# Optimization experiments

Hardware: AMD Instinct MI355X
Metric: run time of the kernel (lower is better)

Reference implementation:

```python
import jax, jax.numpy as jnp
import numpy as np

STRIDES = (2, 2, 1)   # module init arg: (2,2,1) per docstring example
EPS = 1e-5            # InstanceNorm epsilon
ALPHA = 0.2           # leaky relu slope
DN = ('NDHWC', 'DHWIO', 'NDHWC')


def setup_inputs() -> dict:
    key = jax.random.key(0)
    k1, k2 = jax.random.split(key, 2)
    # x: [B, D, H, W, Cin] NDHWC volume batch
    x = jax.random.normal(k1, (4, 128, 128, 32, 32), dtype=jnp.float32)
    # w: per-sample hypernetwork kernels [B, kD, kH, kW, Cin, Cout]
    w = jax.random.normal(k2, (4, 3, 3, 3, 32, 64), dtype=jnp.float32) * 0.05
    # InstanceNorm affine params (learned)
    gamma = jnp.ones((64,), dtype=jnp.float32)
    beta = jnp.zeros((64,), dtype=jnp.float32)
    return {"x": x, "w": w, "gamma": gamma, "beta": beta}


def _per_sample_conv(xi, wi):
    # xi: [D,H,W,Cin], wi: [kD,kH,kW,Cin,Cout] -> [D',H',W',Cout]
    return jax.lax.conv_general_dilated(
        xi[None], wi, window_strides=STRIDES, padding='SAME',
        dimension_numbers=DN)[0]


def reference(x, w, gamma, beta):
    # batched dynamic conv: distinct kernel per sample, vectorized via vmap
    y = jax.vmap(_per_sample_conv)(x, w)          # [B, D', H', W', Cout]
    # InstanceNorm: normalize over spatial dims per sample, per channel
    mu = jnp.mean(y, axis=(1, 2, 3), keepdims=True)
    var = jnp.var(y, axis=(1, 2, 3), keepdims=True)
    y = (y - mu) * jax.lax.rsqrt(var + EPS) * gamma + beta
    # leaky relu alpha=0.2
    return jnp.where(y >= 0, y, ALPHA * y)
```

## Files before the change

kernel.cpp:

```cpp
#include <hip/hip_runtime.h>
#include <hip/hip_bf16.h>

#define B_ 4
#define D_ 128
#define H_ 128
#define W_ 32
#define CI 32
#define CO 64
#define OD 64
#define OH 64
#define OW 32
#define S_SPATIAL (OD*OH*OW)
#define EPS 1e-5f
#define ALPHA 0.2f

#define XR 9
#define XC 34
#define UNITS (4*XR*XC)
#define XSLICEB (UNITS*16)
#define WSLICEB (9*4096)
#define PLANEF (H_*W_*CI)

typedef __attribute__((ext_vector_type(8))) short short8;
typedef __attribute__((ext_vector_type(4))) float f32x4;

__device__ inline short f2bf(float f) {
    return __builtin_bit_cast(short, __float2bfloat16(f));
}

__device__ inline short8 pack8(float4 a, float4 b) {
    short8 r;
    r[0]=f2bf(a.x); r[1]=f2bf(a.y); r[2]=f2bf(a.z); r[3]=f2bf(a.w);
    r[4]=f2bf(b.x); r[5]=f2bf(b.y); r[6]=f2bf(b.z); r[7]=f2bf(b.w);
    return r;
}

__device__ inline void gload16(const void* g, const void* l) {
    __builtin_amdgcn_global_load_lds(
        (const __attribute__((address_space(1))) void*)g,
        (__attribute__((address_space(3))) void*)l, 16, 0, 0);
}

__global__ __launch_bounds__(512) void zero_ws_kernel(float* ws) {
    ws[threadIdx.x] = 0.f;
}

__global__ __launch_bounds__(64) void wprep_kernel(const float* __restrict__ w,
                                                   short* __restrict__ wp) {
    int blk = blockIdx.x;
    int nf  = blk & 3;
    int tb  = blk >> 2;
    int l   = threadIdx.x;
    int l15 = l & 15, lhi = l >> 4;
    const float* wsrc = w + (size_t)tb * (CI*CO);
    short8 v;
#pragma unroll
    for (int j = 0; j < 8; ++j)
        v[j] = f2bf(wsrc[(lhi*8 + j)*CO + nf*16 + l15]);
    *(short8*)(wp + (size_t)blk*512 + l*8) = v;
}

#define BARRIER_FULL() \
    asm volatile("s_waitcnt vmcnt(0) lgkmcnt(0)" ::: "memory"); \
    __builtin_amdgcn_s_barrier(); \
    __builtin_amdgcn_sched_barrier(0)

#define BARRIER_LGKM() \
    asm volatile("s_waitcnt lgkmcnt(0)" ::: "memory"); \
    __builtin_amdgcn_s_barrier(); \
    __builtin_amdgcn_sched_barrier(0)

__global__ __launch_bounds__(256, 2) void conv_mfma_kernel(const float* __restrict__ x,
                                                           const short* __restrict__ wp,
                                                           float* __restrict__ out,
                                                           float* __restrict__ ws) {
    const int bid = blockIdx.x;
    const int b   = bid >> 10;
    const int od  = (bid >> 4) & 63;
    const int oh0 = (bid & 15) << 2;
    const int t   = threadIdx.x;
    const int wv  = t >> 6;
    const int l   = t & 63;
    const int l15 = l & 15;
    const int lhi = l >> 4;

    const float* xb  = x + (size_t)b * (D_*PLANEF);
    const short* wpb = wp + (size_t)b * (27*2048);

    __shared__ __align__(16) char smem[XSLICEB + WSLICEB];
    char* xbuf = smem;
    char* wbuf = smem + XSLICEB;

    int soff[5];
#pragma unroll
    for (int k = 0; k < 5; ++k) {
        int U   = t + (k << 8);
        int g   = U / (XR*XC);
        int rem = U % (XR*XC);
        int r   = rem / XC;
        int c   = rem % XC;
        int ih  = oh0*2 + r;
        int iw  = c - 1;
        soff[k] = (U < UNITS && ih < H_ && (unsigned)iw < (unsigned)W_)
                    ? (ih*(W_*CI) + iw*CI + g*8) : -1;
    }

    f32x4 acc[2][4];
#pragma unroll
    for (int mf = 0; mf < 2; ++mf)
#pragma unroll
        for (int nf = 0; nf < 4; ++nf)
            acc[mf][nf] = (f32x4){0.f, 0.f, 0.f, 0.f};

    auto stage = [&](const float* plane, int kd) {
        const short* wsrc = wpb + (size_t)kd * (9*2048);
#pragma unroll
        for (int k = 0; k < 9; ++k) {
            int u = t + (k << 8);
            gload16(wsrc + u*8, wbuf + u*16);
        }
        float4 la[5], lb[5];
#pragma unroll
        for (int k = 0; k < 5; ++k) {
            if (soff[k] >= 0) {
                la[k] = *(const float4*)(plane + soff[k]);
                lb[k] = *(const float4*)(plane + soff[k] + 4);
            } else {
                la[k] = make_float4(0.f,0.f,0.f,0.f);
                lb[k] = la[k];
            }
        }
#pragma unroll
        for (int k = 0; k < 5; ++k) {
            int U = t + (k << 8);
            if (U < UNITS) *(short8*)(xbuf + U*16) = pack8(la[k], lb[k]);
        }
    };

    auto compute = [&]() {
#pragma unroll
        for (int kh = 0; kh < 3; ++kh) {
            const int r = 2*wv + kh;
#pragma unroll
            for (int kw = 0; kw < 3; ++kw) {
                const char* wpt = wbuf + (kh*3 + kw)*4096 + l*16;
                short8 bf0 = *(const short8*)(wpt);
                short8 bf1 = *(const short8*)(wpt + 1024);
                short8 bf2 = *(const short8*)(wpt + 2048);
                short8 bf3 = *(const short8*)(wpt + 3072);
#pragma unroll
                for (int mf = 0; mf < 2; ++mf) {
                    int c = mf*16 + l15 + kw;
                    int U = (lhi*XR + r)*XC + c;
                    short8 a = *(const short8*)(xbuf + U*16);
                    acc[mf][0] = __builtin_amdgcn_mfma_f32_16x16x32_bf16(a, bf0, acc[mf][0], 0,0,0);
                    acc[mf][1] = __builtin_amdgcn_mfma_f32_16x16x32_bf16(a, bf1, acc[mf][1], 0,0,0);
                    acc[mf][2] = __builtin_amdgcn_mfma_f32_16x16x32_bf16(a, bf2, acc[mf][2], 0,0,0);
                    acc[mf][3] = __builtin_amdgcn_mfma_f32_16x16x32_bf16(a, bf3, acc[mf][3], 0,0,0);
                }
            }
        }
    };

    const int id0 = od*2;
    const float* p0 = xb + (size_t)id0 * PLANEF;
    const float* p1 = p0 + PLANEF;
    const bool has2 = (id0 + 2) < D_;
    const float* p2 = has2 ? (p1 + PLANEF) : p1;

    stage(p0, 0);
    BARRIER_FULL();
    compute();
    BARRIER_LGKM();
    stage(p1, 1);
    BARRIER_FULL();
    compute();
    BARRIER_LGKM();
    stage(p2, 2);
    BARRIER_FULL();
    if (has2) compute();

    const int oh = oh0 + wv;
    float* yb = out + (size_t)((b*OD + od)*OH + oh) * (OW*CO);
#pragma unroll
    for (int mf = 0; mf < 2; ++mf)
#pragma unroll
        for (int nf = 0; nf < 4; ++nf)
#pragma unroll
            for (int r = 0; r < 4; ++r) {
                int ow = mf*16 + lhi*4 + r;
                int co = nf*16 + l15;
                yb[ow*CO + co] = acc[mf][nf][r];
            }

    __syncthreads();
    float* lsum = (float*)smem;
    float* lsq  = (float*)(smem + 1024);
    float csum[4], csq[4];
#pragma unroll
    for (int nf = 0; nf < 4; ++nf) {
        float s = 0.f, q = 0.f;
#pragma unroll
        for (int mf = 0; mf < 2; ++mf)
#pragma unroll
            for (int r = 0; r < 4; ++r) {
                float v = acc[mf][nf][r];
                s += v;
                q = fmaf(v, v, q);
            }
        s += __shfl_xor(s, 16, 64); s += __shfl_xor(s, 32, 64);
        q += __shfl_xor(q, 16, 64); q += __shfl_xor(q, 32, 64);
        csum[nf] = s; csq[nf] = q;
    }
    if (lhi == 0) {
#pragma unroll
        for (int nf = 0; nf < 4; ++nf) {
            lsum[wv*64 + nf*16 + l15] = csum[nf];
            lsq[wv*64 + nf*16 + l15]  = csq[nf];
        }
    }
    __syncthreads();
    if (t < 64) {
        float s = lsum[t] + lsum[64 + t] + lsum[128 + t] + lsum[192 + t];
        float q = lsq[t]  + lsq[64 + t]  + lsq[128 + t]  + lsq[192 + t];
        atomicAdd(&ws[b*64 + t], s);
        atomicAdd(&ws[256 + b*64 + t], q);
    }
}

__global__ __launch_bounds__(256) void finalize_kernel(float* ws,
                                                       const float* __restrict__ gamma,
                                                       const float* __restrict__ beta) {
    int t = threadIdx.x;
    int co = t & 63;
    const float invS = 1.0f / (float)S_SPATIAL;
    float sum = ws[t];
    float sq  = ws[256 + t];
    float mu  = sum * invS;
    float var = sq * invS - mu*mu;
    float scale = rsqrtf(var + EPS) * gamma[co];
    ws[512 + t] = scale;
    ws[768 + t] = beta[co] - mu*scale;
}

__global__ __launch_bounds__(256) void norm_kernel(float* __restrict__ y,
                                                   const float* __restrict__ ws) {
    size_t i = (size_t)blockIdx.x * 256 + threadIdx.x;
    int b = (int)(i >> 21);
    const float4* scp = (const float4*)(ws + 512 + b*64);
    const float4* shp = (const float4*)(ws + 768 + b*64);
    float4 sc = scp[i & 15];
    float4 sh = shp[i & 15];
    float4 v = ((const float4*)y)[i];
    float4 r;
    r.x = fmaf(v.x, sc.x, sh.x);
    r.y = fmaf(v.y, sc.y, sh.y);
    r.z = fmaf(v.z, sc.z, sh.z);
    r.w = fmaf(v.w, sc.w, sh.w);
    r.x = r.x >= 0.f ? r.x : ALPHA * r.x;
    r.y = r.y >= 0.f ? r.y : ALPHA * r.y;
    r.z = r.z >= 0.f ? r.z : ALPHA * r.z;
    r.w = r.w >= 0.f ? r.w : ALPHA * r.w;
    ((float4*)y)[i] = r;
}

extern "C" void kernel_launch(void* const* d_in, const int* in_sizes, int n_in,
                              void* d_out, int out_size, void* d_ws, size_t ws_size,
                              hipStream_t stream) {
    const float* x     = (const float*)d_in[0];
    const float* w     = (const float*)d_in[1];
    const float* gamma = (const float*)d_in[2];
    const float* beta  = (const float*)d_in[3];
    float* out = (float*)d_out;
    float* ws  = (float*)d_ws;
    short* wp  = (short*)((char*)d_ws + 4096);

    zero_ws_kernel<<<1, 512, 0, stream>>>(ws);
    wprep_kernel<<<B_*27*4, 64, 0, stream>>>(w, wp);
    conv_mfma_kernel<<<B_*OD*(OH/4), 256, 0, stream>>>(x, wp, out, ws);
    finalize_kernel<<<1, 256, 0, stream>>>(ws, gamma, beta);
    norm_kernel<<<32768, 256, 0, stream>>>(out, ws);
}
```

Before: 242.4 us.

## Overlap async x-plane DMA with MFMA compute via raw LDS staging and double buffering

Input planes are now fetched with asynchronous global-to-LDS loads of raw fp32 rows into an XOR-swizzled buffer. They are then repacked to bf16 in LDS, double-buffered so the next plane's DMA overlaps the current plane's MFMA work. Weight fragments are read straight from global/L2 instead of being staged through LDS. This hides global load latency behind compute, at the cost of more LDS, possibly lower occupancy, and per-iteration global weight reads.

New measurement: 232.2 us. 4.2% less time.

```diff
diff --git a/kernel.cpp b/kernel.cpp
--- a/kernel.cpp
+++ b/kernel.cpp
@@ -17,9 +17,10 @@
 #define XR 9
 #define XC 34
 #define UNITS (4*XR*XC)
-#define XSLICEB (UNITS*16)
-#define WSLICEB (9*4096)
-#define PLANEF (H_*W_*CI)
+#define BFSLICE (UNITS*16)
+#define ROWF 1024
+#define RAWB (XR*ROWF*4)
+#define PLANEF (H_*ROWF)
 
 typedef __attribute__((ext_vector_type(8))) short short8;
 typedef __attribute__((ext_vector_type(4))) float f32x4;
@@ -60,12 +61,12 @@
     *(short8*)(wp + (size_t)blk*512 + l*8) = v;
 }
 
-#define BARRIER_FULL() \
+#define BAR_VM0() \
     asm volatile("s_waitcnt vmcnt(0) lgkmcnt(0)" ::: "memory"); \
     __builtin_amdgcn_s_barrier(); \
     __builtin_amdgcn_sched_barrier(0)
 
-#define BARRIER_LGKM() \
+#define BAR_LGKM() \
     asm volatile("s_waitcnt lgkmcnt(0)" ::: "memory"); \
     __builtin_amdgcn_s_barrier(); \
     __builtin_amdgcn_sched_barrier(0)
@@ -87,23 +88,43 @@
     const float* xb  = x + (size_t)b * (D_*PLANEF);
     const short* wpb = wp + (size_t)b * (27*2048);
 
-    __shared__ __align__(16) char smem[XSLICEB + WSLICEB];
-    char* xbuf = smem;
-    char* wbuf = smem + XSLICEB;
-
-    int soff[5];
-#pragma unroll
-    for (int k = 0; k < 5; ++k) {
-        int U   = t + (k << 8);
-        int g   = U / (XR*XC);
-        int rem = U % (XR*XC);
-        int r   = rem / XC;
-        int c   = rem % XC;
-        int ih  = oh0*2 + r;
-        int iw  = c - 1;
-        soff[k] = (U < UNITS && ih < H_ && (unsigned)iw < (unsigned)W_)
-                    ? (ih*(W_*CI) + iw*CI + g*8) : -1;
-    }
+    __shared__ __align__(16) char smem[RAWB + 2*BFSLICE];
+    float* raw = (float*)smem;
+    char*  bf0 = smem + RAWB;
+    char*  bf1 = smem + RAWB + BFSLICE;
+
+    const int lnF = (l << 2) ^ ((l & 0x38) >> 1);
+    auto dma_x = [&](const float* plane) {
+#pragma unroll
+        for (int k = 0; k < XR; ++k) {
+            int ih = oh0*2 + k; if (ih > H_-1) ih = H_-1;
+            gload16(plane + (size_t)ih*ROWF + wv*256 + lnF,
+                    raw + k*ROWF + wv*256);
+        }
+    };
+
+    auto repack = [&](char* dst) {
+#pragma unroll
+        for (int k = 0; k < 5; ++k) {
+            int U = t + (k << 8);
+            if (U < UNITS) {
+                int g   = U / (XR*XC);
+                int rem = U % (XR*XC);
+                int r   = rem / XC;
+                int c   = rem % XC;
+                int iw  = c - 1;
+                short8 v = (short8){0,0,0,0,0,0,0,0};
+                if ((unsigned)iw < (unsigned)W_ && (oh0*2 + r) < H_) {
+                    int o  = r*ROWF + iw*32 + g*8;
+                    int sw = (iw & 7) << 2;
+                    float4 a = *(const float4*)(raw + (o ^ sw));
+                    float4 bq = *(const float4*)(raw + ((o + 4) ^ sw));
+                    v = pack8(a, bq);
+                }
+                *(short8*)(dst + U*16) = v;
+            }
+        }
+    };
 
     f32x4 acc[2][4];
 #pragma unroll
@@ -112,73 +133,53 @@
         for (int nf = 0; nf < 4; ++nf)
             acc[mf][nf] = (f32x4){0.f, 0.f, 0.f, 0.f};
 
-    auto stage = [&](const float* plane, int kd) {
-        const short* wsrc = wpb + (size_t)kd * (9*2048);
-#pragma unroll
-        for (int k = 0; k < 9; ++k) {
-            int u = t + (k << 8);
-            gload16(wsrc + u*8, wbuf + u*16);
-        }
-        float4 la[5], lb[5];
-#pragma unroll
-        for (int k = 0; k < 5; ++k) {
-            if (soff[k] >= 0) {
-                la[k] = *(const float4*)(plane + soff[k]);
-                lb[k] = *(const float4*)(plane + soff[k] + 4);
-            } else {
-                la[k] = make_float4(0.f,0.f,0.f,0.f);
-                lb[k] = la[k];
-            }
-        }
-#pragma unroll
-        for (int k = 0; k < 5; ++k) {
-            int U = t + (k << 8);
-            if (U < UNITS) *(short8*)(xbuf + U*16) = pack8(la[k], lb[k]);
-        }
-    };
-
-    auto compute = [&]() {
+    auto compute = [&](int kd, const char* base) {
+        const short* wkd = wpb + (size_t)kd*(9*2048) + l*8;
 #pragma unroll
         for (int kh = 0; kh < 3; ++kh) {
             const int r = 2*wv + kh;
 #pragma unroll
             for (int kw = 0; kw < 3; ++kw) {
-                const char* wpt = wbuf + (kh*3 + kw)*4096 + l*16;
-                short8 bf0 = *(const short8*)(wpt);
-                short8 bf1 = *(const short8*)(wpt + 1024);
-                short8 bf2 = *(const short8*)(wpt + 2048);
-                short8 bf3 = *(const short8*)(wpt + 3072);
+                const short* wpt = wkd + (kh*3 + kw)*2048;
+                short8 bq0 = *(const short8*)(wpt);
+                short8 bq1 = *(const short8*)(wpt + 512);
+                short8 bq2 = *(const short8*)(wpt + 1024);
+                short8 bq3 = *(const short8*)(wpt + 1536);
 #pragma unroll
                 for (int mf = 0; mf < 2; ++mf) {
                     int c = mf*16 + l15 + kw;
                     int U = (lhi*XR + r)*XC + c;
-                    short8 a = *(const short8*)(xbuf + U*16);
-                    acc[mf][0] = __builtin_amdgcn_mfma_f32_16x16x32_bf16(a, bf0, acc[mf][0], 0,0,0);
-                    acc[mf][1] = __builtin_amdgcn_mfma_f32_16x16x32_bf16(a, bf1, acc[mf][1], 0,0,0);
-                    acc[mf][2] = __builtin_amdgcn_mfma_f32_16x16x32_bf16(a, bf2, acc[mf][2], 0,0,0);
-                    acc[mf][3] = __builtin_amdgcn_mfma_f32_16x16x32_bf16(a, bf3, acc[mf][3], 0,0,0);
+                    short8 a = *(const short8*)(base + U*16);
+                    acc[mf][0] = __builtin_amdgcn_mfma_f32_16x16x32_bf16(a, bq0, acc[mf][0], 0,0,0);
+                    acc[mf][1] = __builtin_amdgcn_mfma_f32_16x16x32_bf16(a, bq1, acc[mf][1], 0,0,0);
+                    acc[mf][2] = __builtin_amdgcn_mfma_f32_16x16x32_bf16(a, bq2, acc[mf][2], 0,0,0);
+                    acc[mf][3] = __builtin_amdgcn_mfma_f32_16x16x32_bf16(a, bq3, acc[mf][3], 0,0,0);
                 }
             }
         }
     };
 
     const int id0 = od*2;
+    const bool has2 = (id0 + 2) < D_;
     const float* p0 = xb + (size_t)id0 * PLANEF;
     const float* p1 = p0 + PLANEF;
-    const bool has2 = (id0 + 2) < D_;
     const float* p2 = has2 ? (p1 + PLANEF) : p1;
 
-    stage(p0, 0);
-    BARRIER_FULL();
-    compute();
-    BARRIER_LGKM();
-    stage(p1, 1);
-    BARRIER_FULL();
-    compute();
-    BARRIER_LGKM();
-    stage(p2, 2);
-    BARRIER_FULL();
-    if (has2) compute();
+    dma_x(p0);
+    BAR_VM0();
+    repack(bf0);
+    BAR_LGKM();
+    dma_x(p1);
+    compute(0, bf0);
+    BAR_VM0();
+    repack(bf1);
+    BAR_LGKM();
+    dma_x(p2);
+    compute(1, bf1);
+    BAR_VM0();
+    repack(bf0);
+    BAR_LGKM();
+    if (has2) compute(2, bf0);
 
     const int oh = oh0 + wv;
     float* yb = out + (size_t)((b*OD + od)*OH + oh) * (OW*CO);
```
